# Performance work log

Measured on AMD Instinct MI355X. Metric: run time of the kernel, lower is better.

## Reference

```python
import jax, jax.numpy as jnp
import numpy as np

B, S, D, H = 4, 2048, 1024, 16
DK = D // H

def setup_inputs() -> dict:
    key = jax.random.key(0)
    ks = jax.random.split(key, 5)
    scale = 1.0 / np.sqrt(D)
    return {
        "x": jax.random.normal(ks[0], (B, S, D), dtype=jnp.float32),
        "Wq": jax.random.normal(ks[1], (H, D, DK), dtype=jnp.float32) * scale,
        "Wk": jax.random.normal(ks[2], (H, D, DK), dtype=jnp.float32) * scale,
        "Wv": jax.random.normal(ks[3], (H, D, DK), dtype=jnp.float32) * scale,
        "Wo": jax.random.normal(ks[4], (D, D), dtype=jnp.float32) * scale,
    }

def reference(x, Wq, Wk, Wv, Wo):
    # x: [B,S,D]; Wq/Wk/Wv: [H,D,DK] (stacked per-head Linear weights); Wo: [D,D]
    seq = x.shape[-2]
    q = jnp.einsum('bsd,hdk->bhsk', x, Wq)
    k = jnp.einsum('bsd,hdk->bhsk', x, Wk)
    v = jnp.einsum('bsd,hdk->bhsk', x, Wv)
    dk = q.shape[-1]
    scores = jnp.einsum('bhqk,bhsk->bhqs', q, k) / jnp.sqrt(jnp.asarray(dk, x.dtype))
    # causal mask: mask out strictly-future positions (triu, diagonal=1)
    causal = jnp.tril(jnp.ones((seq, seq), dtype=bool))  # True = keep
    scores = jnp.where(causal, scores, -jnp.inf)
    probs = jax.nn.softmax(scores, axis=-1)  # attn_pdrop = 0.0 -> dropout is identity
    attn = jnp.einsum('bhqs,bhsk->bhqk', probs, v)
    # concat heads: [B,S,H*DK]
    concat = attn.transpose(0, 2, 1, 3).reshape(x.shape[0], seq, -1)
    # output_proj: nn.Linear(D, D, bias=False) -> y = concat @ Wo.T
    return jnp.einsum('bsd,ed->bse', concat, Wo)
```

## Files before the change

kernel.cpp:

```cpp
#include <hip/hip_runtime.h>

#define B_ 4
#define S_ 2048
#define D_ 1024
#define H_ 16
#define DK_ 64

typedef __attribute__((ext_vector_type(8))) short bf16x8;
typedef __attribute__((ext_vector_type(4))) float f32x4;
typedef __attribute__((ext_vector_type(4))) unsigned int u32x4;

__device__ __forceinline__ unsigned short f2bf(float f) {
    unsigned int u = __float_as_uint(f);
    u += 0x7FFFu + ((u >> 16) & 1u);
    return (unsigned short)(u >> 16);
}

__global__ void cvt_kernel(const float* __restrict__ src, unsigned short* __restrict__ dst) {
    int i = (blockIdx.x * 256 + threadIdx.x) * 8;
    float4 f0 = *(const float4*)&src[i];
    float4 f1 = *(const float4*)&src[i + 4];
    unsigned short t[8] __attribute__((aligned(16))) = {
        f2bf(f0.x), f2bf(f0.y), f2bf(f0.z), f2bf(f0.w),
        f2bf(f1.x), f2bf(f1.y), f2bf(f1.z), f2bf(f1.w)};
    *(u32x4*)&dst[i] = *(const u32x4*)t;
}

__global__ void prepack_kernel(const float* __restrict__ Wq,
                               const float* __restrict__ Wk,
                               const float* __restrict__ Wv,
                               unsigned short* __restrict__ Wt) {
    __shared__ unsigned short Ts[64 * 65];
    int h = blockIdx.x, w3 = blockIdx.y, t = blockIdx.z;
    const float* src = (w3 == 0 ? Wq : (w3 == 1 ? Wk : Wv)) + h * D_ * DK_ + t * 64 * DK_;
    unsigned short* dst = Wt + (w3 * H_ + h) * DK_ * D_ + t * 64;
    int tid = threadIdx.x;
    for (int rep = 0; rep < 16; ++rep) {
        int idx = rep * 256 + tid;
        int dl = idx >> 6, k = idx & 63;
        Ts[k * 65 + dl] = f2bf(src[dl * 64 + k]);
    }
    __syncthreads();
    for (int rep = 0; rep < 16; ++rep) {
        int idx = rep * 256 + tid;
        int kl = idx >> 6, dl = idx & 63;
        dst[kl * D_ + dl] = Ts[kl * 65 + dl];
    }
}

__device__ __forceinline__ void stage_tile_async(const unsigned short* __restrict__ g,
                                                 unsigned short* lds_base, int wv, int lane, int K) {
#pragma unroll
    for (int it = 0; it < 4; ++it) {
        int rbase = wv * 32 + it * 8;
        int r = rbase + (lane >> 3);
        int gc = (lane & 7) ^ ((lane >> 3) & 7);
        const unsigned short* gp = g + r * K + gc * 8;
        unsigned short* lp = lds_base + rbase * 64;
        __builtin_amdgcn_global_load_lds((const __attribute__((address_space(1))) unsigned int*)gp,
                                         (__attribute__((address_space(3))) unsigned int*)lp,
                                         16, 0, 0);
    }
}

template <bool QKV_OUT>
__global__ __launch_bounds__(256) void gemm128_kernel(const unsigned short* __restrict__ A,
                                                      const unsigned short* __restrict__ Bt,
                                                      void* __restrict__ Out) {
    __shared__ __align__(16) unsigned short As[128 * 64];
    __shared__ __align__(16) unsigned short Bs[128 * 64];
    const int tid = threadIdx.x;
    const int wv = tid >> 6, lane = tid & 63, l15 = lane & 15, q4 = lane >> 4;
    const int wm = wv >> 1, wn = wv & 1;
    const int r0 = blockIdx.x * 128, c0 = blockIdx.y * 128;

    const unsigned short* Ab = A + r0 * D_;
    const unsigned short* Bb = Bt + c0 * D_;

    f32x4 acc[4][4] = {};

    for (int kt = 0; kt < 16; ++kt) {
        stage_tile_async(Ab + kt * 64, As, wv, lane, D_);
        stage_tile_async(Bb + kt * 64, Bs, wv, lane, D_);
        __syncthreads();
#pragma unroll
        for (int kk = 0; kk < 2; ++kk) {
            bf16x8 af[4], bf[4];
            const int sw = ((kk * 4 + q4) ^ (l15 & 7)) * 8;
#pragma unroll
            for (int i = 0; i < 4; ++i) {
                af[i] = *(const bf16x8*)&As[(wm * 64 + i * 16 + l15) * 64 + sw];
                bf[i] = *(const bf16x8*)&Bs[(wn * 64 + i * 16 + l15) * 64 + sw];
            }
#pragma unroll
            for (int i = 0; i < 4; ++i)
#pragma unroll
                for (int j = 0; j < 4; ++j)
                    acc[i][j] = __builtin_amdgcn_mfma_f32_16x16x32_bf16(af[i], bf[j], acc[i][j], 0, 0, 0);
        }
        __syncthreads();
    }
#pragma unroll
    for (int i = 0; i < 4; ++i)
#pragma unroll
        for (int j = 0; j < 4; ++j)
#pragma unroll
            for (int rr = 0; rr < 4; ++rr) {
                int grow = r0 + wm * 64 + i * 16 + q4 * 4 + rr;
                int gcol = c0 + wn * 64 + j * 16 + l15;
                if (QKV_OUT) {
                    int b = grow >> 11, s = grow & (S_ - 1);
                    int w3 = gcol >> 10, h = (gcol >> 6) & 15, dk = gcol & 63;
                    ((unsigned short*)Out)[(((w3 * B_ + b) * H_ + h) * S_ + s) * DK_ + dk] =
                        f2bf(acc[i][j][rr]);
                } else {
                    ((float*)Out)[grow * D_ + gcol] = acc[i][j][rr];
                }
            }
}

__global__ __launch_bounds__(256) void attn_kernel(const unsigned short* __restrict__ qkv,
                                                   unsigned short* __restrict__ concat) {
    const int pr = blockIdx.x;
    const int h = blockIdx.y, b = blockIdx.z;
    const unsigned short* Qp = qkv + ((0 * B_ + b) * H_ + h) * S_ * DK_;
    const unsigned short* Kp = qkv + ((1 * B_ + b) * H_ + h) * S_ * DK_;
    const unsigned short* Vp = qkv + ((2 * B_ + b) * H_ + h) * S_ * DK_;

    __shared__ __align__(16) unsigned short Ks[64 * 72];
    __shared__ __align__(16) unsigned short Vt[64 * 74];
    __shared__ __align__(16) unsigned short Ps[4][32 * 72];

    const int tid = threadIdx.x;
    const int wv = tid >> 6, lane = tid & 63, l15 = lane & 15, q4 = lane >> 4;

    const float cs = 0.125f * 1.44269504088896340736f;
    const float MB = 16.0f;

    for (int side = 0; side < 2; ++side) {
        const int q0 = (side == 0 ? pr : 15 - pr) * 128;
        const int nk = q0 / 64 + 2;

        bf16x8 aq[2][2];
#pragma unroll
        for (int rt = 0; rt < 2; ++rt)
#pragma unroll
            for (int kk = 0; kk < 2; ++kk)
                aq[rt][kk] = *(const bf16x8*)&Qp[(q0 + wv * 32 + rt * 16 + l15) * DK_ + kk * 32 + q4 * 8];

        f32x4 o[2][4] = {};
        float l_[2][4] = {};

        for (int t = 0; t < nk; ++t) {
            const int k0 = t * 64;
#pragma unroll
            for (int it = 0; it < 2; ++it) {
                int c = it * 256 + tid;
                int row = c >> 3, ch = c & 7;
                *(u32x4*)&Ks[row * 72 + ch * 8] = *(const u32x4*)&Kp[(k0 + row) * DK_ + ch * 8];
                u32x4 vv = *(const u32x4*)&Vp[(k0 + row) * DK_ + ch * 8];
                const unsigned short* pv = (const unsigned short*)&vv;
#pragma unroll
                for (int j = 0; j < 8; ++j) Vt[(ch * 8 + j) * 74 + row] = pv[j];
            }
            __syncthreads();

#pragma unroll
            for (int rt = 0; rt < 2; ++rt) {
                f32x4 sa[4] = {};
#pragma unroll
                for (int kk = 0; kk < 2; ++kk)
#pragma unroll
                    for (int ct = 0; ct < 4; ++ct) {
                        bf16x8 bk = *(const bf16x8*)&Ks[(ct * 16 + l15) * 72 + kk * 32 + q4 * 8];
                        sa[ct] = __builtin_amdgcn_mfma_f32_16x16x32_bf16(aq[rt][kk], bk, sa[ct], 0, 0, 0);
                    }
                const int qrow_base = q0 + wv * 32 + rt * 16 + q4 * 4;
#pragma unroll
                for (int ct = 0; ct < 4; ++ct) {
                    int col = k0 + ct * 16 + l15;
#pragma unroll
                    for (int r = 0; r < 4; ++r) {
                        float arg = sa[ct][r] * cs - MB;
                        arg = (col <= qrow_base + r) ? fminf(arg, 20.0f) : -1000.0f;
                        float p = exp2f(arg);
                        l_[rt][r] += p;
                        Ps[wv][(rt * 16 + q4 * 4 + r) * 72 + ct * 16 + l15] = f2bf(p);
                    }
                }
            }
#pragma unroll
            for (int kk = 0; kk < 2; ++kk) {
                bf16x8 a0 = *(const bf16x8*)&Ps[wv][l15 * 72 + kk * 32 + q4 * 8];
                bf16x8 a1 = *(const bf16x8*)&Ps[wv][(16 + l15) * 72 + kk * 32 + q4 * 8];
#pragma unroll
                for (int cd = 0; cd < 4; ++cd) {
                    bf16x8 bv = *(const bf16x8*)&Vt[(cd * 16 + l15) * 74 + kk * 32 + q4 * 8];
                    o[0][cd] = __builtin_amdgcn_mfma_f32_16x16x32_bf16(a0, bv, o[0][cd], 0, 0, 0);
                    o[1][cd] = __builtin_amdgcn_mfma_f32_16x16x32_bf16(a1, bv, o[1][cd], 0, 0, 0);
                }
            }
            __syncthreads();
        }

#pragma unroll
        for (int rt = 0; rt < 2; ++rt)
#pragma unroll
            for (int r = 0; r < 4; ++r) {
                float lr = l_[rt][r];
                lr += __shfl_xor(lr, 1);
                lr += __shfl_xor(lr, 2);
                lr += __shfl_xor(lr, 4);
                lr += __shfl_xor(lr, 8);
                float inv = 1.0f / fmaxf(lr, 1.0e-37f);
                int row = q0 + wv * 32 + rt * 16 + q4 * 4 + r;
#pragma unroll
                for (int cd = 0; cd < 4; ++cd) {
                    int col = h * DK_ + cd * 16 + l15;
                    concat[(b * S_ + row) * D_ + col] = f2bf(o[rt][cd][r] * inv);
                }
            }
    }
}

extern "C" void kernel_launch(void* const* d_in, const int* in_sizes, int n_in,
                              void* d_out, int out_size, void* d_ws, size_t ws_size,
                              hipStream_t stream) {
    const float* x  = (const float*)d_in[0];
    const float* Wq = (const float*)d_in[1];
    const float* Wk = (const float*)d_in[2];
    const float* Wv = (const float*)d_in[3];
    const float* Wo = (const float*)d_in[4];

    unsigned short* qkv    = (unsigned short*)d_ws;
    unsigned short* Wt     = qkv + 3 * B_ * H_ * S_ * DK_;
    unsigned short* xbf    = Wt + 3 * H_ * DK_ * D_;
    unsigned short* concat = xbf;
    unsigned short* Wobf   = Wt;

    cvt_kernel<<<B_ * S_ * D_ / 2048, 256, 0, stream>>>(x, xbf);
    prepack_kernel<<<dim3(H_, 3, 16), 256, 0, stream>>>(Wq, Wk, Wv, Wt);
    gemm128_kernel<true><<<dim3(B_ * S_ / 128, 3 * H_ * DK_ / 128), 256, 0, stream>>>(xbf, Wt, qkv);
    cvt_kernel<<<D_ * D_ / 2048, 256, 0, stream>>>(Wo, Wobf);
    attn_kernel<<<dim3(8, H_, B_), 256, 0, stream>>>(qkv, concat);
    gemm128_kernel<false><<<dim3(B_ * S_ / 128, D_ / 128), 256, 0, stream>>>(concat, Wobf, d_out);
}
```

Measured before the change: 290.6 us.

## Shrink attention query tile to 64 rows, swizzle V transpose, skip masking off-diagonal

The attention kernel now processes 64-query tiles (16 rows per wave) instead of 128, doubling the grid to 16×H×B blocks with paired causal tiles for load balance. Causal masking is applied only on the diagonal key tile, the V transpose in shared memory uses an XOR swizzle with stride 72 instead of padding 74, and P is converted with packed bf16 intrinsics. Launch bounds request 4 blocks per SM for occupancy. The aim is more parallelism and less per-element mask work. The cost is that each K/V tile is reloaded by twice as many blocks, and each MFMA has less reuse.

New measurement: 279.0 us. 1.04x faster.

```diff
diff --git a/kernel.cpp b/kernel.cpp
--- a/kernel.cpp
+++ b/kernel.cpp
@@ -1,4 +1,5 @@
 #include <hip/hip_runtime.h>
+#include <hip/hip_bf16.h>
 
 #define B_ 4
 #define S_ 2048
@@ -119,8 +120,8 @@
             }
 }
 
-__global__ __launch_bounds__(256) void attn_kernel(const unsigned short* __restrict__ qkv,
-                                                   unsigned short* __restrict__ concat) {
+__global__ __launch_bounds__(256, 4) void attn_kernel(const unsigned short* __restrict__ qkv,
+                                                      unsigned short* __restrict__ concat) {
     const int pr = blockIdx.x;
     const int h = blockIdx.y, b = blockIdx.z;
     const unsigned short* Qp = qkv + ((0 * B_ + b) * H_ + h) * S_ * DK_;
@@ -128,8 +129,8 @@
     const unsigned short* Vp = qkv + ((2 * B_ + b) * H_ + h) * S_ * DK_;
 
     __shared__ __align__(16) unsigned short Ks[64 * 72];
-    __shared__ __align__(16) unsigned short Vt[64 * 74];
-    __shared__ __align__(16) unsigned short Ps[4][32 * 72];
+    __shared__ __align__(16) unsigned short Vt[64 * 72];
+    __shared__ __align__(16) __hip_bfloat16 Ps[4][16 * 72];
 
     const int tid = threadIdx.x;
     const int wv = tid >> 6, lane = tid & 63, l15 = lane & 15, q4 = lane >> 4;
@@ -138,18 +139,16 @@
     const float MB = 16.0f;
 
     for (int side = 0; side < 2; ++side) {
-        const int q0 = (side == 0 ? pr : 15 - pr) * 128;
-        const int nk = q0 / 64 + 2;
-
-        bf16x8 aq[2][2];
-#pragma unroll
-        for (int rt = 0; rt < 2; ++rt)
-#pragma unroll
-            for (int kk = 0; kk < 2; ++kk)
-                aq[rt][kk] = *(const bf16x8*)&Qp[(q0 + wv * 32 + rt * 16 + l15) * DK_ + kk * 32 + q4 * 8];
-
-        f32x4 o[2][4] = {};
-        float l_[2][4] = {};
+        const int q0 = (side == 0 ? pr : 31 - pr) * 64;
+        const int nk = q0 / 64 + 1;
+
+        bf16x8 aq[2];
+#pragma unroll
+        for (int kk = 0; kk < 2; ++kk)
+            aq[kk] = *(const bf16x8*)&Qp[(q0 + wv * 16 + l15) * DK_ + kk * 32 + q4 * 8];
+
+        f32x4 o[4] = {};
+        float l_[4] = {};
 
         for (int t = 0; t < nk; ++t) {
             const int k0 = t * 64;
@@ -161,65 +160,82 @@
                 u32x4 vv = *(const u32x4*)&Vp[(k0 + row) * DK_ + ch * 8];
                 const unsigned short* pv = (const unsigned short*)&vv;
 #pragma unroll
-                for (int j = 0; j < 8; ++j) Vt[(ch * 8 + j) * 74 + row] = pv[j];
+                for (int j = 0; j < 8; ++j)
+                    Vt[(ch * 8 + j) * 72 + (row ^ (ch * 8))] = pv[j];
             }
             __syncthreads();
 
-#pragma unroll
-            for (int rt = 0; rt < 2; ++rt) {
-                f32x4 sa[4] = {};
-#pragma unroll
-                for (int kk = 0; kk < 2; ++kk)
-#pragma unroll
-                    for (int ct = 0; ct < 4; ++ct) {
-                        bf16x8 bk = *(const bf16x8*)&Ks[(ct * 16 + l15) * 72 + kk * 32 + q4 * 8];
-                        sa[ct] = __builtin_amdgcn_mfma_f32_16x16x32_bf16(aq[rt][kk], bk, sa[ct], 0, 0, 0);
+            f32x4 sa[4] = {};
+#pragma unroll
+            for (int kk = 0; kk < 2; ++kk)
+#pragma unroll
+                for (int ct = 0; ct < 4; ++ct) {
+                    bf16x8 bk = *(const bf16x8*)&Ks[(ct * 16 + l15) * 72 + kk * 32 + q4 * 8];
+                    sa[ct] = __builtin_amdgcn_mfma_f32_16x16x32_bf16(aq[kk], bk, sa[ct], 0, 0, 0);
+                }
+
+            if (t < nk - 1) {
+#pragma unroll
+                for (int ct = 0; ct < 4; ++ct)
+#pragma unroll
+                    for (int r = 0; r < 4; r += 2) {
+                        float p0 = exp2f(sa[ct][r] * cs - MB);
+                        float p1 = exp2f(sa[ct][r + 1] * cs - MB);
+                        l_[r] += p0;
+                        l_[r + 1] += p1;
+                        __hip_bfloat162 pk = __float22bfloat162_rn(make_float2(p0, p1));
+                        Ps[wv][(q4 * 4 + r) * 72 + ct * 16 + l15] = pk.x;
+                        Ps[wv][(q4 * 4 + r + 1) * 72 + ct * 16 + l15] = pk.y;
                     }
-                const int qrow_base = q0 + wv * 32 + rt * 16 + q4 * 4;
+            } else {
+                const int qrow_base = q0 + wv * 16 + q4 * 4;
 #pragma unroll
                 for (int ct = 0; ct < 4; ++ct) {
                     int col = k0 + ct * 16 + l15;
 #pragma unroll
-                    for (int r = 0; r < 4; ++r) {
-                        float arg = sa[ct][r] * cs - MB;
-                        arg = (col <= qrow_base + r) ? fminf(arg, 20.0f) : -1000.0f;
-                        float p = exp2f(arg);
-                        l_[rt][r] += p;
-                        Ps[wv][(rt * 16 + q4 * 4 + r) * 72 + ct * 16 + l15] = f2bf(p);
+                    for (int r = 0; r < 4; r += 2) {
+                        float a0 = (col <= qrow_base + r) ? sa[ct][r] * cs - MB : -1000.0f;
+                        float a1 = (col <= qrow_base + r + 1) ? sa[ct][r + 1] * cs - MB : -1000.0f;
+                        float p0 = exp2f(a0);
+                        float p1 = exp2f(a1);
+                        l_[r] += p0;
+                        l_[r + 1] += p1;
+                        __hip_bfloat162 pk = __float22bfloat162_rn(make_float2(p0, p1));
+                        Ps[wv][(q4 * 4 + r) * 72 + ct * 16 + l15] = pk.x;
+                        Ps[wv][(q4 * 4 + r + 1) * 72 + ct * 16 + l15] = pk.y;
                     }
                 }
             }
+
 #pragma unroll
             for (int kk = 0; kk < 2; ++kk) {
-                bf16x8 a0 = *(const bf16x8*)&Ps[wv][l15 * 72 + kk * 32 + q4 * 8];
-                bf16x8 a1 = *(const bf16x8*)&Ps[wv][(16 + l15) * 72 + kk * 32 + q4 * 8];
+                bf16x8 ap = *(const bf16x8*)&Ps[wv][l15 * 72 + kk * 32 + q4 * 8];
 #pragma unroll
                 for (int cd = 0; cd < 4; ++cd) {
-                    bf16x8 bv = *(const bf16x8*)&Vt[(cd * 16 + l15) * 74 + kk * 32 + q4 * 8];
-                    o[0][cd] = __builtin_amdgcn_mfma_f32_16x16x32_bf16(a0, bv, o[0][cd], 0, 0, 0);
-                    o[1][cd] = __builtin_amdgcn_mfma_f32_16x16x32_bf16(a1, bv, o[1][cd], 0, 0, 0);
+                    int drow = cd * 16 + l15;
+                    int kbase = (kk * 32 + q4 * 8) ^ (drow & 56);
+                    bf16x8 bv = *(const bf16x8*)&Vt[drow * 72 + kbase];
+                    o[cd] = __builtin_amdgcn_mfma_f32_16x16x32_bf16(ap, bv, o[cd], 0, 0, 0);
                 }
             }
             __syncthreads();
         }
 
 #pragma unroll
-        for (int rt = 0; rt < 2; ++rt)
-#pragma unroll
-            for (int r = 0; r < 4; ++r) {
-                float lr = l_[rt][r];
-                lr += __shfl_xor(lr, 1);
-                lr += __shfl_xor(lr, 2);
-                lr += __shfl_xor(lr, 4);
-                lr += __shfl_xor(lr, 8);
-                float inv = 1.0f / fmaxf(lr, 1.0e-37f);
-                int row = q0 + wv * 32 + rt * 16 + q4 * 4 + r;
-#pragma unroll
-                for (int cd = 0; cd < 4; ++cd) {
-                    int col = h * DK_ + cd * 16 + l15;
-                    concat[(b * S_ + row) * D_ + col] = f2bf(o[rt][cd][r] * inv);
-                }
-            }
+        for (int r = 0; r < 4; ++r) {
+            float lr = l_[r];
+            lr += __shfl_xor(lr, 1);
+            lr += __shfl_xor(lr, 2);
+            lr += __shfl_xor(lr, 4);
+            lr += __shfl_xor(lr, 8);
+            float inv = 1.0f / fmaxf(lr, 1.0e-37f);
+            int row = q0 + wv * 16 + q4 * 4 + r;
+#pragma unroll
+            for (int cd = 0; cd < 4; ++cd) {
+                int col = h * DK_ + cd * 16 + l15;
+                concat[(b * S_ + row) * D_ + col] = f2bf(o[cd][r] * inv);
+            }
+        }
     }
 }
 
@@ -242,6 +258,6 @@
     prepack_kernel<<<dim3(H_, 3, 16), 256, 0, stream>>>(Wq, Wk, Wv, Wt);
     gemm128_kernel<true><<<dim3(B_ * S_ / 128, 3 * H_ * DK_ / 128), 256, 0, stream>>>(xbf, Wt, qkv);
     cvt_kernel<<<D_ * D_ / 2048, 256, 0, stream>>>(Wo, Wobf);
-    attn_kernel<<<dim3(8, H_, B_), 256, 0, stream>>>(qkv, concat);
+    attn_kernel<<<dim3(16, H_, B_), 256, 0, stream>>>(qkv, concat);
     gemm128_kernel<false><<<dim3(B_ * S_ / 128, D_ / 128), 256, 0, stream>>>(concat, Wobf, d_out);
 }
```
